# Performance work log

Hardware: AMD Instinct MI355X
Metric: run time of the kernel (lower is better)

Reference implementation:

```python
import jax, jax.numpy as jnp
import numpy as np

B, S, D_IN, D_H = 8, 2048, 512, 512

def setup_inputs() -> dict:
    key = jax.random.key(0)
    ks = jax.random.split(key, 7)
    s = 1.0 / np.sqrt(D_IN)
    return {
        "x": jax.random.normal(ks[0], (B, S, D_IN), dtype=jnp.float32),
        "Wq": jax.random.uniform(ks[1], (D_H, D_IN), jnp.float32, -s, s),
        "bq": jax.random.uniform(ks[2], (D_H,), jnp.float32, -s, s),
        "Wk": jax.random.uniform(ks[3], (D_H, D_IN), jnp.float32, -s, s),
        "bk": jax.random.uniform(ks[4], (D_H,), jnp.float32, -s, s),
        "Wv": jax.random.uniform(ks[5], (D_H, D_IN), jnp.float32, -s, s),
        "bv": jax.random.uniform(ks[6], (D_H,), jnp.float32, -s, s),
    }

def reference(x, Wq, bq, Wk, bk, Wv, bv):
    # torch Linear: y = x @ W.T + b
    Q = jnp.einsum('bsd,hd->bsh', x, Wq) + bq
    K = jnp.einsum('bsd,hd->bsh', x, Wk) + bk
    V = jnp.einsum('bsd,hd->bsh', x, Wv) + bv
    scale = jnp.sqrt(jnp.asarray(D_H, dtype=x.dtype))
    scores = jnp.einsum('bqh,bkh->bqk', Q, K) / scale  # [B,S,S]
    attn = jax.nn.softmax(scores, axis=-1)
    return jnp.einsum('bqk,bkh->bqh', attn, V)
```

## Files before the change

### kernel.cpp

```cpp
#include <hip/hip_runtime.h>
#include <hip/hip_bf16.h>
#include <cstdint>

#define B_   8
#define S_   2048
#define DIN  512
#define DH   512

typedef __attribute__((ext_vector_type(8))) short  short8;
typedef __attribute__((ext_vector_type(4))) short  short4_;
typedef __attribute__((ext_vector_type(4))) float  float4_;

__device__ inline unsigned short f2bf(float f) {
    union { float f; unsigned u; } v; v.f = f;
    unsigned u = v.u;
    u += 0x7fffu + ((u >> 16) & 1u);
    return (unsigned short)(u >> 16);
}

__device__ inline void gload_lds16(const void* g, void* l) {
    __builtin_amdgcn_global_load_lds(
        (const __attribute__((address_space(1))) void*)g,
        (__attribute__((address_space(3))) void*)l, 16, 0, 0);
}

template <int C>
__device__ inline float fdpp(float x) {
    return __int_as_float(__builtin_amdgcn_update_dpp(0, __float_as_int(x), C, 0xF, 0xF, true));
}
__device__ inline float rsum16(float v) {
    v += fdpp<0x140>(v);
    v += fdpp<0x141>(v);
    v += fdpp<27>(v);
    v += fdpp<177>(v);
    return v;
}

__global__ __launch_bounds__(256) void conv_bf16(
    const float* __restrict__ x,
    const float* __restrict__ Wq, const float* __restrict__ Wk, const float* __restrict__ Wv,
    unsigned short* __restrict__ xb, unsigned short* __restrict__ wb)
{
    const int NX4 = (B_ * S_ * DIN) / 4;
    const int NW4 = (DH * DIN) / 4;
    const int total = NX4 + 3 * NW4;
    for (int i = blockIdx.x * blockDim.x + threadIdx.x; i < total;
         i += gridDim.x * blockDim.x) {
        const float4_* src; unsigned short* dst; int j;
        if (i < NX4)             { src = (const float4_*)x;  dst = xb;            j = i; }
        else if (i < NX4 + NW4)  { src = (const float4_*)Wq; dst = wb;            j = i - NX4; }
        else if (i < NX4 + 2*NW4){ src = (const float4_*)Wk; dst = wb + DH*DIN;   j = i - NX4 - NW4; }
        else                     { src = (const float4_*)Wv; dst = wb + 2*DH*DIN; j = i - NX4 - 2*NW4; }
        float4_ v = src[j];
        short4_ o;
        o[0] = (short)f2bf(v[0]); o[1] = (short)f2bf(v[1]);
        o[2] = (short)f2bf(v[2]); o[3] = (short)f2bf(v[3]);
        ((short4_*)dst)[j] = o;
    }
}

__global__ __launch_bounds__(256) void qkv_gemm(
    const unsigned short* __restrict__ xb,
    const unsigned short* __restrict__ wb,
    const float* __restrict__ bq, const float* __restrict__ bk, const float* __restrict__ bv,
    unsigned short* __restrict__ qws, unsigned short* __restrict__ kws,
    unsigned short* __restrict__ vt2)
{
    __shared__ __align__(16) unsigned short smem[17408];

    const int tm   = blockIdx.x;
    const int tc   = blockIdx.y;
    const int mat  = tc >> 2;
    const int nb   = (tc & 3) * 128;
    const int tid  = threadIdx.x;
    const int w    = tid >> 6;
    const int lane = tid & 63;
    const int l15  = lane & 15;
    const int quad = lane >> 4;
    const int wm   = (w & 1) * 64;
    const int wn   = (w >> 1) * 64;
    const int m0   = tm * 128;

    const unsigned short* wmat = wb + (size_t)mat * DH * DIN;

    float4_ zero = {0.f, 0.f, 0.f, 0.f};
    float4_ acc[4][4];
    #pragma unroll
    for (int i = 0; i < 4; i++)
        #pragma unroll
        for (int j = 0; j < 4; j++) acc[i][j] = zero;

    const int lr = lane >> 2;
    const int lb = (lane & 3) * 16;

    auto stage = [&](int kk, int bufi) {
        unsigned short* Ab = smem + bufi * 8192;
        unsigned short* Bb = smem + 4096 + bufi * 8192;
        #pragma unroll
        for (int c = 0; c < 2; c++) {
            int r = w * 32 + c * 16;
            const unsigned char* gA = (const unsigned char*)(xb + (size_t)(m0 + r) * DIN + kk);
            gload_lds16(gA + (size_t)lr * (DIN * 2) + lb, (void*)(Ab + r * 32));
            const unsigned char* gB = (const unsigned char*)(wmat + (size_t)(nb + r) * DIN + kk);
            gload_lds16(gB + (size_t)lr * (DIN * 2) + lb, (void*)(Bb + r * 32));
        }
    };

    stage(0, 0);
    for (int ki = 0; ki < 16; ki++) {
        __syncthreads();
        if (ki < 15) stage((ki + 1) * 32, (ki + 1) & 1);
        const unsigned short* Ab = smem + (ki & 1) * 8192;
        const unsigned short* Bb = smem + 4096 + (ki & 1) * 8192;
        short8 af[4], bf[4];
        #pragma unroll
        for (int mt = 0; mt < 4; mt++)
            af[mt] = *(const short8*)(Ab + (wm + mt * 16 + l15) * 32 + quad * 8);
        #pragma unroll
        for (int nt = 0; nt < 4; nt++)
            bf[nt] = *(const short8*)(Bb + (wn + nt * 16 + l15) * 32 + quad * 8);
        #pragma unroll
        for (int mt = 0; mt < 4; mt++)
            #pragma unroll
            for (int nt = 0; nt < 4; nt++)
                acc[mt][nt] = __builtin_amdgcn_mfma_f32_16x16x32_bf16(af[mt], bf[nt], acc[mt][nt], 0, 0, 0);
    }

    if (mat < 2) {
        const float* bias  = (mat == 0) ? bq : bk;
        const float  scale = (mat == 0) ? 0.06375870430742225f : 1.0f;
        unsigned short* dst = (mat == 0) ? qws : kws;
        #pragma unroll
        for (int nt = 0; nt < 4; nt++) {
            int n = nb + wn + nt * 16 + l15;
            float bv_ = bias[n];
            #pragma unroll
            for (int mt = 0; mt < 4; mt++) {
                #pragma unroll
                for (int r = 0; r < 4; r++) {
                    int m = m0 + wm + mt * 16 + quad * 4 + r;
                    dst[(size_t)m * DH + n] = f2bf((acc[mt][nt][r] + bv_) * scale);
                }
            }
        }
    } else {
        __syncthreads();
        unsigned short* trans = smem;
        #pragma unroll
        for (int nt = 0; nt < 4; nt++) {
            int dloc = wn + nt * 16 + l15;
            float bv_ = bv[nb + dloc];
            #pragma unroll
            for (int mt = 0; mt < 4; mt++) {
                short4_ pk;
                #pragma unroll
                for (int r = 0; r < 4; r++) pk[r] = (short)f2bf(acc[mt][nt][r] + bv_);
                *(short4_*)(trans + dloc * 136 + wm + mt * 16 + quad * 4) = pk;
            }
        }
        __syncthreads();
        int dl   = tid >> 1;
        int h    = tid & 1;
        int dh_g = nb + dl;
        int bi   = m0 >> 11;
        int tile0 = (m0 & 2047) >> 4;
        unsigned char* vt2b = (unsigned char*)vt2;
        #pragma unroll
        for (int t = 0; t < 4; t++) {
            int tl = h * 4 + t;
            const uint4* c = (const uint4*)(trans + dl * 136 + tl * 16);
            unsigned char* dst = vt2b + ((size_t)(bi * 128 + tile0 + tl) << 14) + dh_g * 32;
            ((uint4*)dst)[0] = c[0];
            ((uint4*)dst)[1] = c[1];
        }
    }
}

__global__ __launch_bounds__(512, 2) void attn(
    const unsigned short* __restrict__ qws,
    const unsigned short* __restrict__ kws,
    const unsigned short* __restrict__ vt2,
    float* __restrict__ out)
{
    __shared__ __align__(16) unsigned char smem[141824];

    const int bid  = blockIdx.x;
    const int b    = bid & 7;
    const int qt_b = bid >> 3;
    const int tid  = threadIdx.x;
    const int w    = tid >> 6;
    const int g    = w >> 2;
    const int wl   = w & 3;
    const int lane = tid & 63;
    const int l15  = lane & 15;
    const int quad = lane >> 4;

    const int qrow0  = b * S_ + qt_b * 64;
    const int myqrow = qrow0 + wl * 16;

    const unsigned short* kgrp = kws + (size_t)(b * S_ + g * 1024) * DH;
    const unsigned char*  vtb  = (const unsigned char*)vt2;

    unsigned char* kb    = smem + g * 65536;
    unsigned char* vb    = smem + g * 65536 + 32768;
    unsigned char* pbase = smem + 131072 + g * 5120;
    float*         lbuf  = (float*)(smem + 141312);

    short8 qf[16];
    {
        const short8* qp = (const short8*)(qws + (size_t)(myqrow + l15) * DH);
        #pragma unroll
        for (int ksi = 0; ksi < 16; ksi++) qf[ksi] = qp[ksi * 4 + quad];
    }

    float4_ zero = {0.f, 0.f, 0.f, 0.f};
    float4_ o[16];
    #pragma unroll
    for (int i = 0; i < 16; i++) o[i] = zero;
    float l_[4] = {0.f, 0.f, 0.f, 0.f};

    auto stageK = [&](int n, int bufi) {
        #pragma unroll
        for (int i = 0; i < 4; i++) {
            int row = wl * 4 + i;
            const unsigned char* gp =
                (const unsigned char*)(kgrp + (size_t)(n * 16 + row) * DH);
            gload_lds16(gp + ((lane ^ (row & 7)) << 4),
                        kb + bufi * 16384 + row * 1024);
        }
    };
    auto stageV = [&](int n, int bufi) {
        const unsigned char* base =
            vtb + ((size_t)(b * 128 + g * 64 + n) << 14) + wl * 4096;
        #pragma unroll
        for (int i = 0; i < 4; i++)
            gload_lds16(base + i * 1024 + lane * 16,
                        vb + bufi * 16384 + wl * 4096 + i * 1024);
    };

    auto doPV = [&](int bufi) {
        const unsigned char* pq = smem + 131072 + (quad >> 1) * 5120
                                + bufi * 2560 + (quad & 1) * 16;
        const unsigned char* vq = smem + (quad >> 1) * 65536 + 32768
                                + bufi * 16384 + (quad & 1) * 16;
        short8 pa[4];
        #pragma unroll
        for (int qt = 0; qt < 4; qt++)
            pa[qt] = *(const short8*)(pq + (qt * 16 + l15) * 40);
        #pragma unroll
        for (int dht = 0; dht < 4; dht++) {
            short8 vf = *(const short8*)(vq + (size_t)(w * 64 + dht * 16 + l15) * 32);
            #pragma unroll
            for (int qt = 0; qt < 4; qt++)
                o[qt * 4 + dht] = __builtin_amdgcn_mfma_f32_16x16x32_bf16(pa[qt], vf, o[qt * 4 + dht], 0, 0, 0);
        }
    };

    stageK(0, 0);

    for (int it = 0; it < 64; it++) {
        __syncthreads();

        if (it < 63) stageK(it + 1, (it + 1) & 1);
        stageV(it, it & 1);

        const unsigned char* kt_ = kb + (it & 1) * 16384;
        float4_ s0 = zero, s1 = zero;
        #pragma unroll
        for (int ksi = 0; ksi < 16; ksi += 2) {
            short8 k0 = *(const short8*)(kt_ + l15 * 1024 + ((( ksi      * 4 + quad) ^ (l15 & 7)) << 4));
            short8 k1 = *(const short8*)(kt_ + l15 * 1024 + ((((ksi + 1) * 4 + quad) ^ (l15 & 7)) << 4));
            s0 = __builtin_amdgcn_mfma_f32_16x16x32_bf16(qf[ksi],     k0, s0, 0, 0, 0);
            s1 = __builtin_amdgcn_mfma_f32_16x16x32_bf16(qf[ksi + 1], k1, s1, 0, 0, 0);
        }
        float4_ sc = s0 + s1;

        unsigned short* pp = (unsigned short*)(pbase + (it & 1) * 2560);
        #pragma unroll
        for (int r = 0; r < 4; r++) {
            float p = __builtin_exp2f(sc[r]);
            l_[r] += p;
            pp[(wl * 16 + quad * 4 + r) * 20 + l15] = f2bf(p);
        }

        if (it) doPV((it - 1) & 1);
    }

    __syncthreads();
    doPV(1);

    float lsum[4];
    #pragma unroll
    for (int r = 0; r < 4; r++) lsum[r] = rsum16(l_[r]);
    if (l15 == 0) {
        #pragma unroll
        for (int r = 0; r < 4; r++)
            lbuf[g * 64 + wl * 16 + quad * 4 + r] = lsum[r];
    }
    __syncthreads();

    #pragma unroll
    for (int qt = 0; qt < 4; qt++) {
        float rl[4];
        #pragma unroll
        for (int r = 0; r < 4; r++) {
            int row = qt * 16 + quad * 4 + r;
            rl[r] = 1.f / (lbuf[row] + lbuf[64 + row]);
        }
        #pragma unroll
        for (int dht = 0; dht < 4; dht++)
            #pragma unroll
            for (int r = 0; r < 4; r++) {
                int row = qt * 16 + quad * 4 + r;
                out[(size_t)(qrow0 + row) * DH + w * 64 + dht * 16 + l15] =
                    o[qt * 4 + dht][r] * rl[r];
            }
    }
}

extern "C" void kernel_launch(void* const* d_in, const int* in_sizes, int n_in,
                              void* d_out, int out_size, void* d_ws, size_t ws_size,
                              hipStream_t stream) {
    const float* x  = (const float*)d_in[0];
    const float* Wq = (const float*)d_in[1];
    const float* bq = (const float*)d_in[2];
    const float* Wk = (const float*)d_in[3];
    const float* bk = (const float*)d_in[4];
    const float* Wv = (const float*)d_in[5];
    const float* bv = (const float*)d_in[6];
    float* out = (float*)d_out;

    unsigned short* qws = (unsigned short*)d_ws;
    unsigned short* kws = qws + (size_t)B_ * S_ * DH;
    unsigned short* vt2 = kws + (size_t)B_ * S_ * DH;

    unsigned short* xb = (unsigned short*)d_out;
    unsigned short* wb = xb + (size_t)B_ * S_ * DIN;

    conv_bf16<<<dim3(2048), dim3(256), 0, stream>>>(x, Wq, Wk, Wv, xb, wb);
    qkv_gemm<<<dim3(128, 12), dim3(256), 0, stream>>>(xb, wb, bq, bk, bv, qws, kws, vt2);
    attn<<<dim3(256), dim3(512), 0, stream>>>(qws, kws, vt2, out);
}
```

Baseline: 262.5 us.

## Split attention keys into four groups and load V directly into registers

```diff
diff --git a/kernel.cpp b/kernel.cpp
--- a/kernel.cpp
+++ b/kernel.cpp
@@ -68,8 +68,10 @@
 {
     __shared__ __align__(16) unsigned short smem[17408];
 
-    const int tm   = blockIdx.x;
-    const int tc   = blockIdx.y;
+    const int flat = blockIdx.y * 128 + blockIdx.x;
+    const int swz  = (flat & 7) * 192 + (flat >> 3);
+    const int tm   = swz / 12;
+    const int tc   = swz % 12;
     const int mat  = tc >> 2;
     const int nb   = (tc & 3) * 128;
     const int tid  = threadIdx.x;
@@ -182,120 +184,124 @@
     const unsigned short* __restrict__ vt2,
     float* __restrict__ out)
 {
-    __shared__ __align__(16) unsigned char smem[141824];
+    __shared__ __align__(16) unsigned char smem[152576];
 
     const int bid  = blockIdx.x;
     const int b    = bid & 7;
     const int qt_b = bid >> 3;
     const int tid  = threadIdx.x;
     const int w    = tid >> 6;
-    const int g    = w >> 2;
-    const int wl   = w & 3;
+    const int g    = w >> 1;
+    const int h    = w & 1;
     const int lane = tid & 63;
     const int l15  = lane & 15;
     const int quad = lane >> 4;
 
-    const int qrow0  = b * S_ + qt_b * 64;
-    const int myqrow = qrow0 + wl * 16;
-
-    const unsigned short* kgrp = kws + (size_t)(b * S_ + g * 1024) * DH;
+    const int qrow0 = b * S_ + qt_b * 64;
+
+    const unsigned short* kgrp = kws + (size_t)(b * S_ + g * 512) * DH;
     const unsigned char*  vtb  = (const unsigned char*)vt2;
 
-    unsigned char* kb    = smem + g * 65536;
-    unsigned char* vb    = smem + g * 65536 + 32768;
+    unsigned char* kb    = smem + g * 32768;
     unsigned char* pbase = smem + 131072 + g * 5120;
-    float*         lbuf  = (float*)(smem + 141312);
-
-    short8 qf[16];
-    {
-        const short8* qp = (const short8*)(qws + (size_t)(myqrow + l15) * DH);
-        #pragma unroll
-        for (int ksi = 0; ksi < 16; ksi++) qf[ksi] = qp[ksi * 4 + quad];
+    float*         lbuf  = (float*)(smem + 151552);
+
+    short8 qf[2][16];
+    #pragma unroll
+    for (int qi = 0; qi < 2; qi++) {
+        const short8* qp = (const short8*)(qws + (size_t)(qrow0 + h * 32 + qi * 16 + l15) * DH);
+        #pragma unroll
+        for (int ksi = 0; ksi < 16; ksi++) qf[qi][ksi] = qp[ksi * 4 + quad];
     }
 
     float4_ zero = {0.f, 0.f, 0.f, 0.f};
     float4_ o[16];
     #pragma unroll
     for (int i = 0; i < 16; i++) o[i] = zero;
-    float l_[4] = {0.f, 0.f, 0.f, 0.f};
-
-    auto stageK = [&](int n, int bufi) {
-        #pragma unroll
-        for (int i = 0; i < 4; i++) {
-            int row = wl * 4 + i;
+    float l_[8];
+    #pragma unroll
+    for (int i = 0; i < 8; i++) l_[i] = 0.f;
+
+    short8 vreg[8];
+
+    auto stageK = [&](int n, int par) {
+        #pragma unroll
+        for (int i = 0; i < 8; i++) {
+            int row = h * 8 + i;
             const unsigned char* gp =
                 (const unsigned char*)(kgrp + (size_t)(n * 16 + row) * DH);
             gload_lds16(gp + ((lane ^ (row & 7)) << 4),
-                        kb + bufi * 16384 + row * 1024);
+                        kb + par * 16384 + row * 1024);
         }
     };
-    auto stageV = [&](int n, int bufi) {
-        const unsigned char* base =
-            vtb + ((size_t)(b * 128 + g * 64 + n) << 14) + wl * 4096;
-        #pragma unroll
-        for (int i = 0; i < 4; i++)
-            gload_lds16(base + i * 1024 + lane * 16,
-                        vb + bufi * 16384 + wl * 4096 + i * 1024);
+
+    auto loadV = [&](int n) {
+        #pragma unroll
+        for (int dht = 0; dht < 4; dht++)
+            #pragma unroll
+            for (int c = 0; c < 2; c++) {
+                int gc = 2 * c + (quad >> 1);
+                const unsigned char* a = vtb
+                    + ((size_t)(b * 128 + gc * 32 + n) << 14)
+                    + (size_t)(w * 64 + dht * 16 + l15) * 32 + (quad & 1) * 16;
+                vreg[dht * 2 + c] = *(const short8*)a;
+            }
     };
 
-    auto doPV = [&](int bufi) {
-        const unsigned char* pq = smem + 131072 + (quad >> 1) * 5120
-                                + bufi * 2560 + (quad & 1) * 16;
-        const unsigned char* vq = smem + (quad >> 1) * 65536 + 32768
-                                + bufi * 16384 + (quad & 1) * 16;
-        short8 pa[4];
-        #pragma unroll
-        for (int qt = 0; qt < 4; qt++)
-            pa[qt] = *(const short8*)(pq + (qt * 16 + l15) * 40);
-        #pragma unroll
-        for (int dht = 0; dht < 4; dht++) {
-            short8 vf = *(const short8*)(vq + (size_t)(w * 64 + dht * 16 + l15) * 32);
-            #pragma unroll
-            for (int qt = 0; qt < 4; qt++)
-                o[qt * 4 + dht] = __builtin_amdgcn_mfma_f32_16x16x32_bf16(pa[qt], vf, o[qt * 4 + dht], 0, 0, 0);
+    auto doPV = [&](int par) {
+        #pragma unroll
+        for (int qt = 0; qt < 4; qt++) {
+            const int po = (qt * 16 + l15) * 40 + (quad & 1) * 16;
+            short8 pa0 = *(const short8*)(smem + 131072 + ( (quad >> 1)     ) * 5120 + par * 2560 + po);
+            short8 pa1 = *(const short8*)(smem + 131072 + (2 + (quad >> 1)) * 5120 + par * 2560 + po);
+            #pragma unroll
+            for (int dht = 0; dht < 4; dht++) {
+                o[qt * 4 + dht] = __builtin_amdgcn_mfma_f32_16x16x32_bf16(pa0, vreg[dht * 2 + 0], o[qt * 4 + dht], 0, 0, 0);
+                o[qt * 4 + dht] = __builtin_amdgcn_mfma_f32_16x16x32_bf16(pa1, vreg[dht * 2 + 1], o[qt * 4 + dht], 0, 0, 0);
+            }
         }
     };
 
     stageK(0, 0);
 
-    for (int it = 0; it < 64; it++) {
+    for (int it = 0; it < 32; it++) {
         __syncthreads();
 
-        if (it < 63) stageK(it + 1, (it + 1) & 1);
-        stageV(it, it & 1);
+        if (it) loadV(it - 1);
+        if (it < 31) stageK(it + 1, (it + 1) & 1);
 
         const unsigned char* kt_ = kb + (it & 1) * 16384;
-        float4_ s0 = zero, s1 = zero;
-        #pragma unroll
-        for (int ksi = 0; ksi < 16; ksi += 2) {
-            short8 k0 = *(const short8*)(kt_ + l15 * 1024 + ((( ksi      * 4 + quad) ^ (l15 & 7)) << 4));
-            short8 k1 = *(const short8*)(kt_ + l15 * 1024 + ((((ksi + 1) * 4 + quad) ^ (l15 & 7)) << 4));
-            s0 = __builtin_amdgcn_mfma_f32_16x16x32_bf16(qf[ksi],     k0, s0, 0, 0, 0);
-            s1 = __builtin_amdgcn_mfma_f32_16x16x32_bf16(qf[ksi + 1], k1, s1, 0, 0, 0);
-        }
-        float4_ sc = s0 + s1;
+        float4_ sA = zero, sB = zero;
+        #pragma unroll
+        for (int ksi = 0; ksi < 16; ksi++) {
+            short8 kf = *(const short8*)(kt_ + l15 * 1024 + (((ksi * 4 + quad) ^ (l15 & 7)) << 4));
+            sA = __builtin_amdgcn_mfma_f32_16x16x32_bf16(qf[0][ksi], kf, sA, 0, 0, 0);
+            sB = __builtin_amdgcn_mfma_f32_16x16x32_bf16(qf[1][ksi], kf, sB, 0, 0, 0);
+        }
 
         unsigned short* pp = (unsigned short*)(pbase + (it & 1) * 2560);
         #pragma unroll
         for (int r = 0; r < 4; r++) {
-            float p = __builtin_exp2f(sc[r]);
-            l_[r] += p;
-            pp[(wl * 16 + quad * 4 + r) * 20 + l15] = f2bf(p);
+            float p0 = __builtin_exp2f(sA[r]);
+            l_[r] += p0;
+            pp[(h * 32 + quad * 4 + r) * 20 + l15] = f2bf(p0);
+            float p1 = __builtin_exp2f(sB[r]);
+            l_[4 + r] += p1;
+            pp[(h * 32 + 16 + quad * 4 + r) * 20 + l15] = f2bf(p1);
         }
 
         if (it) doPV((it - 1) & 1);
     }
 
     __syncthreads();
+    loadV(31);
     doPV(1);
 
-    float lsum[4];
-    #pragma unroll
-    for (int r = 0; r < 4; r++) lsum[r] = rsum16(l_[r]);
-    if (l15 == 0) {
-        #pragma unroll
-        for (int r = 0; r < 4; r++)
-            lbuf[g * 64 + wl * 16 + quad * 4 + r] = lsum[r];
+    #pragma unroll
+    for (int i = 0; i < 8; i++) {
+        float s = rsum16(l_[i]);
+        if (l15 == 0)
+            lbuf[g * 64 + h * 32 + (i >> 2) * 16 + quad * 4 + (i & 3)] = s;
     }
     __syncthreads();
 
@@ -305,7 +311,7 @@
         #pragma unroll
         for (int r = 0; r < 4; r++) {
             int row = qt * 16 + quad * 4 + r;
-            rl[r] = 1.f / (lbuf[row] + lbuf[64 + row]);
+            rl[r] = 1.f / (lbuf[row] + lbuf[64 + row] + lbuf[128 + row] + lbuf[192 + row]);
         }
         #pragma unroll
         for (int dht = 0; dht < 4; dht++)
```

New measurement: 306.5 us. 1.17x slower.
